# Kernel optimization log

Measured on AMD Instinct MI355X. Metric: run time of the kernel, lower is better.

Reference implementation:

```python
import jax, jax.numpy as jnp
import numpy as np
from jax import lax

HID = 512
NEG = -1e30

def conv2d(x, w, pad):
    # x: [N,C,H,W], w: [O,I,kh,kw]
    return lax.conv_general_dilated(x, w, (1, 1), [(pad, pad), (pad, pad)],
                                    dimension_numbers=('NCHW', 'OIHW', 'NCHW'))

def maxpool3s2p1(x):
    return lax.reduce_window(x, -jnp.inf, lax.max, (1, 1, 3, 3), (1, 1, 2, 2),
                             [(0, 0), (0, 0), (1, 1), (1, 1)])

def setup_inputs() -> dict:
    key = jax.random.key(0)
    ks = jax.random.split(key, 12)
    N, B = 128, 16
    gid = jnp.repeat(jnp.arange(B), N // B).astype(jnp.float32)  # sorted group ids
    rois = jnp.concatenate([gid[:, None], jax.random.uniform(ks[0], (N, 4))], axis=1)
    interact_feat = jax.random.normal(ks[1], (N, 2304, 1, 16, 16), jnp.float32)
    bbox_feat = jax.random.normal(ks[2], (N, 1024, 4, 7, 7), jnp.float32)
    s = lambda k, sh: jax.random.normal(k, sh, jnp.float32) * 0.02
    return {
        'rois': rois,
        'interact_feat': interact_feat,
        'bbox_feat': bbox_feat,
        'w_reduce': s(ks[3], (HID, 2304, 1, 1)),
        'w_rsize': s(ks[4], (HID, HID, 3, 3)),
        'wq': s(ks[5], (HID, HID, 3, 3)),
        'wk': s(ks[6], (HID, HID, 3, 3)),
        'wv': s(ks[7], (HID, HID, 3, 3)),
        'w1': s(ks[8], (HID, HID, 3, 3)),
        'gamma': jnp.ones((HID,), jnp.float32),
        'beta': jnp.zeros((HID,), jnp.float32),
        'w_fc': s(ks[9], (HID, 2 * HID)),
    }

def reference(rois, interact_feat, bbox_feat, w_reduce, w_rsize, wq, wk, wv, w1, gamma, beta, w_fc):
    f = interact_feat[:, :, 0]                      # squeeze(2): [N,2304,16,16]
    f = jax.nn.relu(conv2d(f, w_reduce, 0))         # [N,512,16,16]
    f = conv2d(f, w_rsize, 0)                       # no padding -> [N,512,14,14]
    f = maxpool3s2p1(f)                             # [N,512,7,7]

    gid = rois[:, 0].astype(jnp.int32)
    mask = gid[:, None] == gid[None, :]             # [N,N] same-group mask (vectorizes ragged loop)

    q = conv2d(f, wq, 1)
    k = conv2d(f, wk, 1)
    v = conv2d(f, wv, 1)
    # per-pixel attention across rois within each group
    att = jnp.einsum('ichw,jchw->ijhw', q, k) / jnp.sqrt(jnp.asarray(HID, f.dtype))
    att = jnp.where(mask[:, :, None, None], att, NEG)
    att = jax.nn.softmax(att, axis=1)               # softmax over key rois (dim=1)
    virt = jnp.einsum('ijhw,jchw->ichw', att, v)    # [N,512,7,7]

    # GroupNorm(1, C): normalize over (C,H,W), per-channel affine
    mu = virt.mean(axis=(1, 2, 3), keepdims=True)
    var = virt.var(axis=(1, 2, 3), keepdims=True)
    virt = (virt - mu) / jnp.sqrt(var + 1e-5)
    virt = virt * gamma[None, :, None, None] + beta[None, :, None, None]
    virt = jax.nn.relu(virt)
    virt = conv2d(virt, w1, 1)                      # dropout = identity in eval

    ho = (f + virt).mean(axis=(2, 3))               # gap1 -> [N,512]
    ob = bbox_feat.mean(axis=(2, 3, 4))             # gap2 -> [N,1024]
    ob = jax.nn.relu(ob @ w_fc.T)                   # fc1 -> [N,512]
    return jnp.concatenate([ho, ob], axis=1)        # [N,1024]
```

## Files before the change

### kernel.cpp

```cpp
#include <hip/hip_runtime.h>
#include <hip/hip_bf16.h>
#include <math.h>

typedef __bf16 bf16;
typedef __bf16 v8bf __attribute__((ext_vector_type(8)));
typedef float f32x4 __attribute__((ext_vector_type(4)));

#define GLDS16(g, l) __builtin_amdgcn_global_load_lds( \
    (const __attribute__((address_space(1))) void*)(g), \
    (__attribute__((address_space(3))) void*)(l), 16, 0, 0)

__device__ __forceinline__ int xcd_swz(int bid, int nwg) {
  int xcd = bid & 7, off = bid >> 3;
  int q = nwg >> 3, r = nwg & 7;
  return (xcd < r ? xcd * (q + 1) : r * (q + 1) + (xcd - r) * q) + off;
}

__device__ __forceinline__ void tile_compute(const char* ldsA, const char* ldsB,
                                             f32x4 (&acc)[4][4], int wr, int wc, int lane) {
  const int l15 = lane & 15;
  const int colb = (lane >> 4) << 4;
  #pragma unroll
  for (int kk = 0; kk < 2; ++kk) {
    v8bf a[4], b[4];
    #pragma unroll
    for (int i = 0; i < 4; ++i) {
      int ra = wr * 64 + i * 16 + l15;
      int ca = ((kk << 6) | colb) ^ ((ra & 7) << 4);
      a[i] = *(const v8bf*)(ldsA + ra * 128 + ca);
    }
    #pragma unroll
    for (int j = 0; j < 4; ++j) {
      int rb = wc * 64 + j * 16 + l15;
      int cb = ((kk << 6) | colb) ^ ((rb & 7) << 4);
      b[j] = *(const v8bf*)(ldsB + rb * 128 + cb);
    }
    __builtin_amdgcn_s_setprio(1);
    #pragma unroll
    for (int i = 0; i < 4; ++i)
      #pragma unroll
      for (int j = 0; j < 4; ++j)
        acc[i][j] = __builtin_amdgcn_mfma_f32_16x16x32_bf16(a[i], b[j], acc[i][j], 0, 0, 0);
    __builtin_amdgcn_s_setprio(0);
  }
}

#define PIPELINE_LOOP(NK)                                                   \
  stage(0, lds);                                                            \
  stage(1, lds + 32768);                                                    \
  int cur = 0;                                                              \
  for (int ks = 0; ks < (NK) - 1; ++ks) {                                   \
    asm volatile("s_waitcnt vmcnt(8)" ::: "memory");                        \
    __builtin_amdgcn_s_barrier();                                           \
    __builtin_amdgcn_sched_barrier(0);                                      \
    tile_compute(lds + cur * 32768, lds + cur * 32768 + 16384, acc, wr, wc, lane); \
    __builtin_amdgcn_sched_barrier(0);                                      \
    __builtin_amdgcn_s_barrier();                                           \
    __builtin_amdgcn_sched_barrier(0);                                      \
    if (ks + 2 < (NK)) stage(ks + 2, lds + cur * 32768);                    \
    cur ^= 1;                                                               \
  }                                                                         \
  asm volatile("s_waitcnt vmcnt(0)" ::: "memory");                          \
  __builtin_amdgcn_s_barrier();                                             \
  __builtin_amdgcn_sched_barrier(0);                                        \
  tile_compute(lds + cur * 32768, lds + cur * 32768 + 16384, acc, wr, wc, lane);

template<typename OutT, bool RELU>
__device__ __forceinline__ void store_tile(OutT* __restrict__ C, int m0, int c0,
                                           f32x4 (&acc)[4][4], int lane) {
  const int rbase = (lane >> 4) << 2;
  const int cl = lane & 15;
  #pragma unroll
  for (int i = 0; i < 4; ++i)
    #pragma unroll
    for (int j = 0; j < 4; ++j)
      #pragma unroll
      for (int r = 0; r < 4; ++r) {
        float v = acc[i][j][r];
        if (RELU) v = fmaxf(v, 0.f);
        C[(size_t)(m0 + i * 16 + rbase + r) * 512 + (c0 + j * 16 + cl)] = (OutT)v;
      }
}

__global__ __launch_bounds__(256)
void k_gemm_reduce(const bf16* __restrict__ A, const bf16* __restrict__ B,
                   bf16* __restrict__ f1, int mbase)
{
  __shared__ __attribute__((aligned(16))) char lds[65536];
  const int s = xcd_swz(blockIdx.x, gridDim.x);
  const int by = s & 3, bx = s >> 2;
  const int t = threadIdx.x, lane = t & 63, w = t >> 6, wr = w >> 1, wc = w & 1;
  const int tr = t >> 3;
  const int cphys = ((t & 7) << 4) ^ ((tr & 7) << 4);
  const char* pa[4]; const char* pb[4];
  #pragma unroll
  for (int i = 0; i < 4; ++i) {
    int r = i * 32 + tr;
    pa[i] = (const char*)A + (size_t)(bx * 128 + r) * 4608 + cphys;
    pb[i] = (const char*)B + (size_t)(by * 128 + r) * 4608 + cphys;
  }
  const int lo = t * 16;
  auto stage = [&](int ks, char* base) {
    #pragma unroll
    for (int i = 0; i < 4; ++i) GLDS16(pa[i] + ks * 128, base + lo + i * 4096);
    #pragma unroll
    for (int i = 0; i < 4; ++i) GLDS16(pb[i] + ks * 128, base + 16384 + lo + i * 4096);
  };
  f32x4 acc[4][4] = {};
  PIPELINE_LOOP(36)
  store_tile<bf16, true>(f1, mbase + bx * 128 + wr * 64, by * 128 + wc * 64, acc, lane);
}

__global__ __launch_bounds__(256)
void k_conv_rsize(const bf16* __restrict__ f1, const bf16* __restrict__ wt,
                  bf16* __restrict__ f14)
{
  __shared__ __attribute__((aligned(16))) char lds[65536];
  const int s = xcd_swz(blockIdx.x, gridDim.x);
  const int by = s & 3, bx = s >> 2;
  const int t = threadIdx.x, lane = t & 63, w = t >> 6, wr = w >> 1, wc = w & 1;
  const int tr = t >> 3;
  const int cphys = ((t & 7) << 4) ^ ((tr & 7) << 4);
  int abase[4]; const char* pb[4];
  #pragma unroll
  for (int i = 0; i < 4; ++i) {
    int r = i * 32 + tr;
    int m = bx * 128 + r;
    int n = m / 196, rem = m - n * 196;
    int y = rem / 14, x = rem - 14 * (rem / 14);
    abase[i] = n * 256 + y * 16 + x;
    pb[i] = (const char*)wt + (size_t)(by * 128 + r) * 1024 + cphys;
  }
  const char* f1c = (const char*)f1 + cphys;
  const int lo = t * 16;
  auto stage = [&](int ks, char* base) {
    int tap = ks >> 3, ko = (ks & 7) << 7;
    int dy = (tap * 11) >> 5, dx = tap - dy * 3;
    int doff = dy * 16 + dx;
    #pragma unroll
    for (int i = 0; i < 4; ++i)
      GLDS16(f1c + ((size_t)(abase[i] + doff) << 10) + ko, base + lo + i * 4096);
    #pragma unroll
    for (int i = 0; i < 4; ++i)
      GLDS16(pb[i] + (size_t)tap * 524288 + ko, base + 16384 + lo + i * 4096);
  };
  f32x4 acc[4][4] = {};
  PIPELINE_LOOP(72)
  store_tile<bf16, false>(f14, bx * 128 + wr * 64, by * 128 + wc * 64, acc, lane);
}

__global__ __launch_bounds__(256)
void k_conv_qkv(const bf16* __restrict__ fin, const bf16* __restrict__ wt,
                bf16* __restrict__ qkv, const bf16* __restrict__ zp,
                const float* __restrict__ bbox, float* __restrict__ obm)
{
  __shared__ __attribute__((aligned(16))) char lds[65536];
  const int t = threadIdx.x;
  if (blockIdx.x >= 588) {
    int bid = blockIdx.x - 588;
    int n = bid >> 4;
    int c = (bid & 15) * 64 + (t >> 2);
    int seg = t & 3;
    const float4* p4 = (const float4*)(bbox + ((size_t)n * 1024 + c) * 196);
    float s = 0.f;
    for (int k = seg; k < 49; k += 4) { float4 w = p4[k]; s += w.x + w.y + w.z + w.w; }
    s += __shfl_xor(s, 1);
    s += __shfl_xor(s, 2);
    if (seg == 0) obm[n * 1024 + c] = s * (1.f / 196.f);
    return;
  }
  const int s = xcd_swz(blockIdx.x, 588);
  const int q12 = s % 12, bx = s / 12;
  const int tensor = q12 >> 2, by = q12 & 3;
  const char* wtc = (const char*)wt + (size_t)tensor * 4718592;
  bf16* outp = qkv + (size_t)tensor * 3211264;
  const int lane = t & 63, w = t >> 6, wr = w >> 1, wc = w & 1;
  const int tr = t >> 3;
  const int cphys = ((t & 7) << 4) ^ ((tr & 7) << 4);
  int nb[4], py[4], px[4]; const char* pb[4];
  #pragma unroll
  for (int i = 0; i < 4; ++i) {
    int r = i * 32 + tr;
    int m = bx * 128 + r;
    int n = m / 49, rem = m - n * 49;
    nb[i] = n * 49;
    py[i] = rem / 7 - 1;
    px[i] = rem - 7 * (rem / 7) - 1;
    pb[i] = wtc + (size_t)(by * 128 + r) * 1024 + cphys;
  }
  const char* finc = (const char*)fin + cphys;
  const char* zpc = (const char*)zp;
  const int lo = t * 16;
  auto stage = [&](int ks, char* base) {
    int tap = ks >> 3, ko = (ks & 7) << 7;
    int dy = (tap * 11) >> 5, dx = tap - dy * 3;
    #pragma unroll
    for (int i = 0; i < 4; ++i) {
      int iy = py[i] + dy, ix = px[i] + dx;
      const char* src = ((unsigned)iy < 7u && (unsigned)ix < 7u)
          ? finc + ((size_t)(nb[i] + iy * 7 + ix) << 10) + ko : zpc;
      GLDS16(src, base + lo + i * 4096);
    }
    #pragma unroll
    for (int i = 0; i < 4; ++i)
      GLDS16(pb[i] + (size_t)tap * 524288 + ko, base + 16384 + lo + i * 4096);
  };
  f32x4 acc[4][4] = {};
  PIPELINE_LOOP(72)
  store_tile<bf16, false>(outp, bx * 128 + wr * 64, by * 128 + wc * 64, acc, lane);
}

__global__ __launch_bounds__(256)
void k_gemm_s(const bf16* __restrict__ A_s, const bf16* __restrict__ w1r,
              float* __restrict__ part)
{
  __shared__ __attribute__((aligned(16))) char lds[65536];
  const int by = blockIdx.x, kspl = blockIdx.y;
  const int t = threadIdx.x, lane = t & 63, w = t >> 6, wr = w >> 1, wc = w & 1;
  const int tr = t >> 3;
  const int cphys = ((t & 7) << 4) ^ ((tr & 7) << 4);
  const char* pa[4]; const char* pb[4];
  #pragma unroll
  for (int i = 0; i < 4; ++i) {
    int r = i * 32 + tr;
    pa[i] = (const char*)A_s + (size_t)r * 9216 + kspl * 2304 + cphys;
    pb[i] = (const char*)w1r + (size_t)(by * 128 + r) * 9216 + kspl * 2304 + cphys;
  }
  const int lo = t * 16;
  auto stage = [&](int ks, char* base) {
    #pragma unroll
    for (int i = 0; i < 4; ++i) GLDS16(pa[i] + ks * 128, base + lo + i * 4096);
    #pragma unroll
    for (int i = 0; i < 4; ++i) GLDS16(pb[i] + ks * 128, base + 16384 + lo + i * 4096);
  };
  f32x4 acc[4][4] = {};
  PIPELINE_LOOP(18)
  const int rb = (lane >> 4) << 2, cl = lane & 15;
  #pragma unroll
  for (int i = 0; i < 4; ++i)
    #pragma unroll
    for (int j = 0; j < 4; ++j)
      #pragma unroll
      for (int r = 0; r < 4; ++r) {
        int row = wr * 64 + i * 16 + rb + r;
        int col = by * 128 + wc * 64 + j * 16 + cl;
        part[(size_t)kspl * 65536 + row * 512 + col] = acc[i][j][r];
      }
}

__global__ __launch_bounds__(512)
void k_red(const float* __restrict__ part, const float* __restrict__ f7m,
           float* __restrict__ out)
{
  int idx = blockIdx.x * 512 + threadIdx.x;
  float s = part[idx] + part[65536 + idx] + part[131072 + idx] + part[196608 + idx];
  int row = idx >> 9, col = idx & 511;
  out[row * 1024 + col] = s + f7m[idx];
}

__global__ void k_tin(const float* __restrict__ in, bf16* __restrict__ A1, int n0)
{
  __shared__ float tile[64][36];
  const int k0 = blockIdx.x * 64, p0 = blockIdx.y * 32, nl = blockIdx.z;
  const int n = n0 + nl;
  const int t = threadIdx.x;
  const float* src = in + (size_t)n * 2304 * 256;
  #pragma unroll
  for (int rep = 0; rep < 2; ++rep) {
    int idx = t + rep * 256;
    int row = idx >> 3, c4 = (idx & 7) * 4;
    float4 v = *(const float4*)(src + (size_t)(k0 + row) * 256 + p0 + c4);
    tile[row][c4] = v.x; tile[row][c4 + 1] = v.y;
    tile[row][c4 + 2] = v.z; tile[row][c4 + 3] = v.w;
  }
  __syncthreads();
  const int pl = t >> 3, ke = (t & 7) * 8;
  v8bf o;
  #pragma unroll
  for (int e = 0; e < 8; ++e) o[e] = (bf16)tile[ke + e][pl];
  bf16* dst = A1 + (size_t)nl * 256 * 2304;
  *(v8bf*)(dst + (size_t)(p0 + pl) * 2304 + k0 + ke) = o;
}

__global__ void k_castw(const float* __restrict__ wsrc, bf16* __restrict__ wb, int nelem)
{
  int idx = (blockIdx.x * 256 + threadIdx.x) * 4;
  if (idx >= nelem) return;
  float4 v = *(const float4*)(wsrc + idx);
  bf16 o0 = (bf16)v.x, o1 = (bf16)v.y, o2 = (bf16)v.z, o3 = (bf16)v.w;
  bf16* d = wb + idx;
  d[0] = o0; d[1] = o1; d[2] = o2; d[3] = o3;
}

__global__ void k_wtrans(const float* __restrict__ s0, const float* __restrict__ s1,
                         const float* __restrict__ s2, const float* __restrict__ s3,
                         const float* __restrict__ s4, bf16* __restrict__ wt,
                         bf16* __restrict__ w1r)
{
  const float* src;
  switch (blockIdx.y) {
    case 0: src = s0; break; case 1: src = s1; break; case 2: src = s2; break;
    case 3: src = s3; break; default: src = s4; break;
  }
  int q = blockIdx.x * 256 + threadIdx.x;
  const float* sp = src + (size_t)q * 9;
  float tmp[9];
  #pragma unroll
  for (int e = 0; e < 9; ++e) tmp[e] = sp[e];
  if (blockIdx.y < 4) {
    bf16* dst = wt + (size_t)blockIdx.y * 2359296;
    #pragma unroll
    for (int e = 0; e < 9; ++e) dst[(size_t)e * 262144 + q] = (bf16)tmp[e];
  } else {
    int co = q >> 9, ci = q & 511;
    #pragma unroll
    for (int e = 0; e < 9; ++e) w1r[(size_t)(co * 9 + e) * 512 + ci] = (bf16)tmp[e];
  }
}

__global__ void k_pool(const bf16* __restrict__ f14, bf16* __restrict__ f7b)
{
  int idx = blockIdx.x * 256 + threadIdx.x;
  int c2 = idx & 255;
  int pp = idx >> 8;
  int n = pp / 49, p7 = pp - n * 49;
  int y = p7 / 7, x = p7 - 7 * (p7 / 7);
  int y0 = 2 * y - 1, x0 = 2 * x - 1;
  const unsigned* f14u = (const unsigned*)f14;
  float m0 = -3.4e38f, m1 = -3.4e38f;
  #pragma unroll
  for (int dy = 0; dy < 3; ++dy) {
    int iy = y0 + dy; if ((unsigned)iy >= 14u) continue;
    #pragma unroll
    for (int dx = 0; dx < 3; ++dx) {
      int ix = x0 + dx; if ((unsigned)ix >= 14u) continue;
      unsigned vv = f14u[(size_t)(n * 196 + iy * 14 + ix) * 256 + c2];
      m0 = fmaxf(m0, __builtin_bit_cast(float, vv << 16));
      m1 = fmaxf(m1, __builtin_bit_cast(float, vv & 0xffff0000u));
    }
  }
  bf16 b0 = (bf16)m0, b1 = (bf16)m1;
  unsigned pk = (unsigned)__builtin_bit_cast(unsigned short, b0)
              | ((unsigned)__builtin_bit_cast(unsigned short, b1) << 16);
  ((unsigned*)f7b)[idx] = pk;
}

__global__ __launch_bounds__(256)
void k_attn(const bf16* __restrict__ q, const bf16* __restrict__ k,
            const bf16* __restrict__ v, const float* __restrict__ rois,
            float* __restrict__ virt)
{
  const int p = blockIdx.x, g = blockIdx.y, t = threadIdx.x;
  __shared__ float sS[8][9];
  __shared__ float sP[8][9];
  __shared__ __attribute__((aligned(16))) bf16 sV[8][512];
  {
    int u = t;
    #pragma unroll
    for (int rep = 0; rep < 2; ++rep, u += 256) {
      int j = u >> 6, ch = u & 63;
      *(v8bf*)&sV[j][ch * 8] = *(const v8bf*)(v + ((size_t)(g * 8 + j) * 49 + p) * 512 + ch * 8);
    }
  }
  int pi = t >> 2, ls = t & 3;
  int i = pi >> 3, j = pi & 7;
  const bf16* qi = q + ((size_t)(g * 8 + i) * 49 + p) * 512;
  const bf16* kj = k + ((size_t)(g * 8 + j) * 49 + p) * 512;
  float s = 0.f;
  for (int ch = ls * 16; ch < ls * 16 + 16; ++ch) {
    v8bf a = *(const v8bf*)(qi + ch * 8);
    v8bf b = *(const v8bf*)(kj + ch * 8);
    #pragma unroll
    for (int e = 0; e < 8; ++e) s += (float)a[e] * (float)b[e];
  }
  s += __shfl_xor(s, 1);
  s += __shfl_xor(s, 2);
  if (ls == 0) sS[i][j] = s * 0.04419417382415922f;
  __syncthreads();
  if (t < 8) {
    float gi = rois[(g * 8 + t) * 5];
    float pv[8]; float mx = -3.4e38f;
    #pragma unroll
    for (int jj = 0; jj < 8; ++jj) {
      float gj = rois[(g * 8 + jj) * 5];
      float sv = (gi == gj) ? sS[t][jj] : -1e30f;
      pv[jj] = sv; mx = fmaxf(mx, sv);
    }
    float sum = 0.f;
    #pragma unroll
    for (int jj = 0; jj < 8; ++jj) { float e = expf(pv[jj] - mx); pv[jj] = e; sum += e; }
    float inv = 1.f / sum;
    #pragma unroll
    for (int jj = 0; jj < 8; ++jj) sP[t][jj] = pv[jj] * inv;
  }
  __syncthreads();
  int i2 = t >> 5, c0 = (t & 31) * 16;
  float o[16];
  #pragma unroll
  for (int e = 0; e < 16; ++e) o[e] = 0.f;
  #pragma unroll
  for (int jj = 0; jj < 8; ++jj) {
    float ww = sP[i2][jj];
    v8bf v0 = *(const v8bf*)&sV[jj][c0];
    v8bf v1 = *(const v8bf*)&sV[jj][c0 + 8];
    #pragma unroll
    for (int e = 0; e < 8; ++e) { o[e] += ww * (float)v0[e]; o[8 + e] += ww * (float)v1[e]; }
  }
  float* dst = virt + ((size_t)(g * 8 + i2) * 49 + p) * 512 + c0;
  #pragma unroll
  for (int e = 0; e < 16; ++e) dst[e] = o[e];
}

__global__ __launch_bounds__(512)
void k_ln_fc(const float* __restrict__ virt, const float* __restrict__ gamma,
             const float* __restrict__ beta, const bf16* __restrict__ f7b,
             bf16* __restrict__ A_s, float* __restrict__ f7m,
             const float* __restrict__ obm, const float* __restrict__ wfc,
             float* __restrict__ out)
{
  const int t = threadIdx.x;
  if (blockIdx.x >= 128) {
    __shared__ float sO[1024];
    int n = blockIdx.x - 128;
    for (int u = t; u < 1024; u += 512) sO[u] = obm[n * 1024 + u];
    __syncthreads();
    const float4* wp = (const float4*)(wfc + (size_t)t * 1024);
    float s = 0.f;
    for (int c4 = 0; c4 < 256; ++c4) {
      float4 w = wp[c4];
      s += w.x * sO[c4 * 4] + w.y * sO[c4 * 4 + 1] + w.z * sO[c4 * 4 + 2] + w.w * sO[c4 * 4 + 3];
    }
    out[n * 1024 + 512 + t] = fmaxf(s, 0.f);
    return;
  }
  const int n = blockIdx.x;
  const float* p = virt + (size_t)n * 25088 + t;
  float xv[49];
  float s1 = 0.f, s2 = 0.f;
  #pragma unroll
  for (int pp = 0; pp < 49; ++pp) {
    float x = p[pp * 512];
    xv[pp] = x; s1 += x; s2 += x * x;
  }
  __shared__ float r1[512], r2[512];
  r1[t] = s1; r2[t] = s2; __syncthreads();
  for (int off = 256; off; off >>= 1) {
    if (t < off) { r1[t] += r1[t + off]; r2[t] += r2[t + off]; }
    __syncthreads();
  }
  float mu = r1[0] * (1.f / 25088.f);
  float var = r2[0] * (1.f / 25088.f) - mu * mu;
  float rstd = rsqrtf(var + 1e-5f);
  float g = gamma[t], be = beta[t];
  const bf16* fp = f7b + (size_t)n * 25088 + t;
  float T = 0, R0 = 0, R6 = 0, C0 = 0, C6 = 0;
  float X00 = 0, X06 = 0, X60 = 0, X66 = 0, F = 0;
  #pragma unroll
  for (int pp = 0; pp < 49; ++pp) {
    const int u = pp / 7, v = pp - 7 * (pp / 7);
    float y = fmaxf((xv[pp] - mu) * rstd * g + be, 0.f);
    T += y;
    if (u == 0) R0 += y;
    if (u == 6) R6 += y;
    if (v == 0) C0 += y;
    if (v == 6) C6 += y;
    if (pp == 0)  X00 = y;
    if (pp == 6)  X06 = y;
    if (pp == 42) X60 = y;
    if (pp == 48) X66 = y;
    F += (float)fp[pp * 512];
  }
  float sv[9] = { T-R6-C6+X66, T-R6, T-R6-C0+X60,
                  T-C6,        T,    T-C0,
                  T-R0-C6+X06, T-R0, T-R0-C0+X00 };
  bf16* Ap = A_s + (size_t)n * 4608 + t;
  #pragma unroll
  for (int tap = 0; tap < 9; ++tap)
    Ap[tap * 512] = (bf16)(sv[tap] * (1.f / 49.f));
  f7m[n * 512 + t] = F * (1.f / 49.f);
}

extern "C" void kernel_launch(void* const* d_in, const int* in_sizes, int n_in,
                              void* d_out, int out_size, void* d_ws, size_t ws_size,
                              hipStream_t stream) {
  const float* rois     = (const float*)d_in[0];
  const float* interact = (const float*)d_in[1];
  const float* bbox     = (const float*)d_in[2];
  const float* w_reduce = (const float*)d_in[3];
  const float* w_rsize  = (const float*)d_in[4];
  const float* wq       = (const float*)d_in[5];
  const float* wk       = (const float*)d_in[6];
  const float* wv       = (const float*)d_in[7];
  const float* w1       = (const float*)d_in[8];
  const float* gamma    = (const float*)d_in[9];
  const float* beta     = (const float*)d_in[10];
  const float* wfc      = (const float*)d_in[11];
  float* out = (float*)d_out;
  char* ws = (char*)d_ws;

  size_t o = 0;
  auto take = [&](size_t sz) { size_t r = o; o += (sz + 255) & ~(size_t)255; return r; };
  bf16*  wrb   = (bf16*)(ws + take(2359296));
  bf16*  wt    = (bf16*)(ws + take(18874368));
  bf16*  w1r   = (bf16*)(ws + take(4718592));
  char*  Rf1   = ws + take(33554432);
  bf16*  f7b   = (bf16*)(ws + take(6422528));
  float* virt  = (float*)(ws + take(12845056));
  bf16*  A_s   = (bf16*)(ws + take(1179648));
  float* f7m   = (float*)(ws + take(262144));
  float* part  = (float*)(ws + take(1048576));
  float* obm   = (float*)(ws + take(524288));
  bf16*  zp    = (bf16*)(ws + take(256));
  size_t fixedEnd = o;
  const size_t A1_FULL = 150994944;
  bool full = (ws_size >= fixedEnd + A1_FULL);
  bf16* A1  = (bf16*)(ws + fixedEnd);
  bf16* f14 = (bf16*)(ws + fixedEnd);

  bf16* f1 = (bf16*)Rf1;
  bf16* qb = (bf16*)Rf1;
  bf16* kb = qb + 3211264;
  bf16* vb = kb + 3211264;

  hipMemsetAsync(zp, 0, 256, stream);

  k_castw<<<1152, 256, 0, stream>>>(w_reduce, wrb, 1179648);
  k_wtrans<<<dim3(1024, 5), 256, 0, stream>>>(w_rsize, wq, wk, wv, w1, wt, w1r);

  if (full) {
    k_tin<<<dim3(36, 8, 128), 256, 0, stream>>>(interact, A1, 0);
    k_gemm_reduce<<<1024, 256, 0, stream>>>(A1, wrb, f1, 0);
  } else {
    for (int ch = 0; ch < 4; ++ch) {
      k_tin<<<dim3(36, 8, 32), 256, 0, stream>>>(interact, A1, ch * 32);
      k_gemm_reduce<<<256, 256, 0, stream>>>(A1, wrb, f1, ch * 8192);
    }
  }

  k_conv_rsize<<<784, 256, 0, stream>>>(f1, wt, f14);
  k_pool<<<6272, 256, 0, stream>>>(f14, f7b);

  k_conv_qkv<<<2636, 256, 0, stream>>>(f7b, wt + (size_t)1 * 2359296, qb, zp, bbox, obm);

  k_attn<<<dim3(49, 16), 256, 0, stream>>>(qb, kb, vb, rois, virt);

  k_ln_fc<<<256, 512, 0, stream>>>(virt, gamma, beta, f7b, A_s, f7m, obm, wfc, out);

  k_gemm_s<<<dim3(4, 4), 256, 0, stream>>>(A_s, w1r, part);
  k_red<<<128, 512, 0, stream>>>(part, f7m, out);
}
```

Baseline: 552.1 us.

## Switch main GEMM/conv kernels to 256x256 tiles with 8 waves and 4-stage ring

```diff
diff --git a/kernel.cpp b/kernel.cpp
--- a/kernel.cpp
+++ b/kernel.cpp
@@ -14,6 +14,229 @@
   int xcd = bid & 7, off = bid >> 3;
   int q = nwg >> 3, r = nwg & 7;
   return (xcd < r ? xcd * (q + 1) : r * (q + 1) + (xcd - r) * q) + off;
+}
+
+#define LDA256(ih) do { \
+  _Pragma("unroll") for (int _i = 0; _i < 4; ++_i) { \
+    int _r = (ih) * 64 + _i * 16 + l15; \
+    int _c = (wm * 64 + colb) ^ ((l15 & 7) << 4); \
+    af[_i] = *(const v8bf*)(ringp + _r * 128 + _c); } } while (0)
+
+#define LDB256() do { \
+  _Pragma("unroll") for (int _j = 0; _j < 4; ++_j) { \
+    int _r = (wn & 1) * 64 + _j * 16 + l15; \
+    int _c = ((wn >> 1) * 64 + colb) ^ ((l15 & 7) << 4); \
+    bfr[_j] = *(const v8bf*)(ringp + 16384 + _r * 128 + _c); } } while (0)
+
+#define MMA256(ih) do { \
+  __builtin_amdgcn_s_setprio(1); \
+  _Pragma("unroll") for (int _i = 0; _i < 4; ++_i) \
+  _Pragma("unroll") for (int _j = 0; _j < 4; ++_j) \
+    acc[(ih)*4+_i][_j] = __builtin_amdgcn_mfma_f32_16x16x32_bf16(af[_i], bfr[_j], acc[(ih)*4+_i][_j], 0, 0, 0); \
+  __builtin_amdgcn_s_setprio(0); } while (0)
+
+#define GROUP256(g, NT, STAGEA, STAGEB) do { \
+  const char* ringp = lds + ((g) & 3) * 32768; \
+  char* srng = lds + (((g) + 3) & 3) * 32768; \
+  (void)srng; \
+  const bool _st = ((g) + 3 < (NT)); \
+  LDA256(0); LDB256(); \
+  if (_st) { STAGEA; } \
+  __builtin_amdgcn_s_barrier(); \
+  __builtin_amdgcn_sched_barrier(0); \
+  MMA256(0); \
+  __builtin_amdgcn_sched_barrier(0); \
+  __builtin_amdgcn_s_barrier(); \
+  LDA256(1); \
+  if (_st) { STAGEB; } \
+  if (_st)                       asm volatile("s_waitcnt vmcnt(8)" ::: "memory"); \
+  else if ((g) + 3 == (NT))      asm volatile("s_waitcnt vmcnt(4)" ::: "memory"); \
+  else if ((g) + 3 == (NT) + 1)  asm volatile("s_waitcnt vmcnt(0)" ::: "memory"); \
+  __builtin_amdgcn_s_barrier(); \
+  __builtin_amdgcn_sched_barrier(0); \
+  MMA256(1); \
+  __builtin_amdgcn_sched_barrier(0); \
+  __builtin_amdgcn_s_barrier(); } while (0)
+
+__global__ __launch_bounds__(512, 2)
+void k_gemm_reduce(const bf16* __restrict__ A, const bf16* __restrict__ B,
+                   bf16* __restrict__ f1, int mbase)
+{
+  __shared__ __attribute__((aligned(16))) char lds[131072];
+  const int s = xcd_swz(blockIdx.x, gridDim.x);
+  const int by = s & 1, bx = s >> 1;
+  const int t = threadIdx.x, lane = t & 63, w = t >> 6;
+  const int wm = w >> 2, wn = w & 3;
+  const int l15 = lane & 15, colb = (lane >> 4) << 4;
+  const int tr = t >> 3;
+  const int lb = ((t & 7) << 4) ^ ((tr & 7) << 4);
+  const int hi = lb >> 6, kb = lb & 63;
+  const int t16 = t * 16;
+  const char* pa[2]; const char* pb[2];
+  #pragma unroll
+  for (int j = 0; j < 2; ++j) {
+    pa[j] = (const char*)A + (size_t)(bx * 256 + j * 64 + tr + hi * 128) * 4608 + kb;
+    pb[j] = (const char*)B + (size_t)(by * 256 + j * 64 + tr + hi * 128) * 4608 + kb;
+  }
+  #define SA_GR(kt, ring) do { GLDS16(pa[0]+(size_t)(kt)*64, (ring)+t16); \
+                               GLDS16(pa[1]+(size_t)(kt)*64, (ring)+8192+t16); } while (0)
+  #define SB_GR(kt, ring) do { GLDS16(pb[0]+(size_t)(kt)*64, (ring)+16384+t16); \
+                               GLDS16(pb[1]+(size_t)(kt)*64, (ring)+24576+t16); } while (0)
+  f32x4 acc[8][4] = {};
+  v8bf af[4], bfr[4];
+  SA_GR(0, lds);         SB_GR(0, lds);
+  SA_GR(1, lds + 32768); SB_GR(1, lds + 32768);
+  SA_GR(2, lds + 65536); SB_GR(2, lds + 65536);
+  asm volatile("s_waitcnt vmcnt(8)" ::: "memory");
+  __builtin_amdgcn_s_barrier();
+  for (int g = 0; g < 72; ++g) {
+    GROUP256(g, 72, SA_GR(g + 3, srng), SB_GR(g + 3, srng));
+  }
+  const int rbase = (lane >> 4) << 2, cl = lane & 15;
+  #pragma unroll
+  for (int i = 0; i < 8; ++i)
+    #pragma unroll
+    for (int j = 0; j < 4; ++j)
+      #pragma unroll
+      for (int r = 0; r < 4; ++r) {
+        int row = mbase + bx * 256 + wm * 128 + i * 16 + rbase + r;
+        int col = by * 256 + wn * 64 + j * 16 + cl;
+        f1[(size_t)row * 512 + col] = (bf16)fmaxf(acc[i][j][r], 0.f);
+      }
+}
+
+__global__ __launch_bounds__(512, 2)
+void k_conv_rsize(const bf16* __restrict__ f1, const bf16* __restrict__ wt,
+                  bf16* __restrict__ f14)
+{
+  __shared__ __attribute__((aligned(16))) char lds[131072];
+  const int s = xcd_swz(blockIdx.x, gridDim.x);
+  const int by = s & 1, bx = s >> 1;
+  const int t = threadIdx.x, lane = t & 63, w = t >> 6;
+  const int wm = w >> 2, wn = w & 3;
+  const int l15 = lane & 15, colb = (lane >> 4) << 4;
+  const int tr = t >> 3;
+  const int lb = ((t & 7) << 4) ^ ((tr & 7) << 4);
+  const int hi = lb >> 6, kb = lb & 63;
+  const int t16 = t * 16;
+  int abase[2]; const char* pb[2];
+  #pragma unroll
+  for (int j = 0; j < 2; ++j) {
+    int m = bx * 256 + j * 64 + tr + hi * 128;
+    int n = m / 196, rem = m - n * 196;
+    int y = rem / 14, x = rem - 14 * (rem / 14);
+    abase[j] = n * 256 + y * 16 + x;
+    pb[j] = (const char*)wt + (size_t)(by * 256 + j * 64 + tr + hi * 128) * 1024 + kb;
+  }
+  const char* f1c = (const char*)f1 + kb;
+  #define SA_CR(kt, ring) do { int _tap = (kt) >> 4, _ko = ((kt) & 15) << 6; \
+    int _dy = (_tap * 11) >> 5, _dx = _tap - _dy * 3; int _df = _dy * 16 + _dx; \
+    GLDS16(f1c + (size_t)(abase[0] + _df) * 1024 + _ko, (ring)+t16); \
+    GLDS16(f1c + (size_t)(abase[1] + _df) * 1024 + _ko, (ring)+8192+t16); } while (0)
+  #define SB_CR(kt, ring) do { int _tap = (kt) >> 4, _ko = ((kt) & 15) << 6; \
+    GLDS16(pb[0] + (size_t)_tap * 524288 + _ko, (ring)+16384+t16); \
+    GLDS16(pb[1] + (size_t)_tap * 524288 + _ko, (ring)+24576+t16); } while (0)
+  f32x4 acc[8][4] = {};
+  v8bf af[4], bfr[4];
+  SA_CR(0, lds);         SB_CR(0, lds);
+  SA_CR(1, lds + 32768); SB_CR(1, lds + 32768);
+  SA_CR(2, lds + 65536); SB_CR(2, lds + 65536);
+  asm volatile("s_waitcnt vmcnt(8)" ::: "memory");
+  __builtin_amdgcn_s_barrier();
+  for (int g = 0; g < 144; ++g) {
+    GROUP256(g, 144, SA_CR(g + 3, srng), SB_CR(g + 3, srng));
+  }
+  const int rbase = (lane >> 4) << 2, cl = lane & 15;
+  #pragma unroll
+  for (int i = 0; i < 8; ++i)
+    #pragma unroll
+    for (int j = 0; j < 4; ++j)
+      #pragma unroll
+      for (int r = 0; r < 4; ++r) {
+        int row = bx * 256 + wm * 128 + i * 16 + rbase + r;
+        int col = by * 256 + wn * 64 + j * 16 + cl;
+        f14[(size_t)row * 512 + col] = (bf16)acc[i][j][r];
+      }
+}
+
+__global__ __launch_bounds__(512, 2)
+void k_conv_qkv(const bf16* __restrict__ fin, const bf16* __restrict__ wt,
+                bf16* __restrict__ qkv, const bf16* __restrict__ zp,
+                const float* __restrict__ bbox, float* __restrict__ obm)
+{
+  __shared__ __attribute__((aligned(16))) char lds[131072];
+  const int t = threadIdx.x;
+  if (blockIdx.x >= 150) {
+    int bid = blockIdx.x - 150;
+    int n = bid >> 3;
+    int c = (bid & 7) * 128 + (t >> 2);
+    int seg = t & 3;
+    const float4* p4 = (const float4*)(bbox + ((size_t)n * 1024 + c) * 196);
+    float sum = 0.f;
+    for (int k = seg; k < 49; k += 4) { float4 ww = p4[k]; sum += ww.x + ww.y + ww.z + ww.w; }
+    sum += __shfl_xor(sum, 1);
+    sum += __shfl_xor(sum, 2);
+    if (seg == 0) obm[n * 1024 + c] = sum * (1.f / 196.f);
+    return;
+  }
+  const int s = xcd_swz(blockIdx.x, 150);
+  const int q6 = s % 6, bx = s / 6;
+  const int tensor = q6 >> 1, byl = q6 & 1;
+  const char* wtc = (const char*)wt + (size_t)tensor * 4718592;
+  bf16* outp = qkv + (size_t)tensor * 3211264;
+  const int lane = t & 63, w = t >> 6;
+  const int wm = w >> 2, wn = w & 3;
+  const int l15 = lane & 15, colb = (lane >> 4) << 4;
+  const int tr = t >> 3;
+  const int lb = ((t & 7) << 4) ^ ((tr & 7) << 4);
+  const int hi = lb >> 6, kb = lb & 63;
+  const int t16 = t * 16;
+  int nb[2], py[2], px[2]; const char* pb[2];
+  #pragma unroll
+  for (int j = 0; j < 2; ++j) {
+    int m = bx * 256 + j * 64 + tr + hi * 128;
+    if (m > 6271) m = 6271;
+    int n = m / 49, rem = m - n * 49;
+    nb[j] = n * 49;
+    py[j] = rem / 7 - 1;
+    px[j] = rem - 7 * (rem / 7) - 1;
+    pb[j] = wtc + (size_t)(byl * 256 + j * 64 + tr + hi * 128) * 1024 + kb;
+  }
+  const char* finc = (const char*)fin + kb;
+  const char* zpc = (const char*)zp;
+  #define SA_QK(kt, ring) do { int _tap = (kt) >> 4, _ko = ((kt) & 15) << 6; \
+    int _dy = (_tap * 11) >> 5, _dx = _tap - _dy * 3; \
+    _Pragma("unroll") for (int _j = 0; _j < 2; ++_j) { \
+      int _iy = py[_j] + _dy, _ix = px[_j] + _dx; \
+      const char* _sp = ((unsigned)_iy < 7u && (unsigned)_ix < 7u) \
+          ? finc + (size_t)(nb[_j] + _iy * 7 + _ix) * 1024 + _ko : zpc; \
+      GLDS16(_sp, (ring) + _j * 8192 + t16); } } while (0)
+  #define SB_QK(kt, ring) do { int _tap = (kt) >> 4, _ko = ((kt) & 15) << 6; \
+    GLDS16(pb[0] + (size_t)_tap * 524288 + _ko, (ring)+16384+t16); \
+    GLDS16(pb[1] + (size_t)_tap * 524288 + _ko, (ring)+24576+t16); } while (0)
+  f32x4 acc[8][4] = {};
+  v8bf af[4], bfr[4];
+  SA_QK(0, lds);         SB_QK(0, lds);
+  SA_QK(1, lds + 32768); SB_QK(1, lds + 32768);
+  SA_QK(2, lds + 65536); SB_QK(2, lds + 65536);
+  asm volatile("s_waitcnt vmcnt(8)" ::: "memory");
+  __builtin_amdgcn_s_barrier();
+  for (int g = 0; g < 144; ++g) {
+    GROUP256(g, 144, SA_QK(g + 3, srng), SB_QK(g + 3, srng));
+  }
+  const int rbase = (lane >> 4) << 2, cl = lane & 15;
+  #pragma unroll
+  for (int i = 0; i < 8; ++i)
+    #pragma unroll
+    for (int j = 0; j < 4; ++j)
+      #pragma unroll
+      for (int r = 0; r < 4; ++r) {
+        int row = bx * 256 + wm * 128 + i * 16 + rbase + r;
+        if (row < 6272) {
+          int col = byl * 256 + wn * 64 + j * 16 + cl;
+          outp[(size_t)row * 512 + col] = (bf16)acc[i][j][r];
+        }
+      }
 }
 
 __device__ __forceinline__ void tile_compute(const char* ldsA, const char* ldsB,
@@ -65,151 +288,6 @@
   __builtin_amdgcn_sched_barrier(0);                                        \
   tile_compute(lds + cur * 32768, lds + cur * 32768 + 16384, acc, wr, wc, lane);
 
-template<typename OutT, bool RELU>
-__device__ __forceinline__ void store_tile(OutT* __restrict__ C, int m0, int c0,
-                                           f32x4 (&acc)[4][4], int lane) {
-  const int rbase = (lane >> 4) << 2;
-  const int cl = lane & 15;
-  #pragma unroll
-  for (int i = 0; i < 4; ++i)
-    #pragma unroll
-    for (int j = 0; j < 4; ++j)
-      #pragma unroll
-      for (int r = 0; r < 4; ++r) {
-        float v = acc[i][j][r];
-        if (RELU) v = fmaxf(v, 0.f);
-        C[(size_t)(m0 + i * 16 + rbase + r) * 512 + (c0 + j * 16 + cl)] = (OutT)v;
-      }
-}
-
-__global__ __launch_bounds__(256)
-void k_gemm_reduce(const bf16* __restrict__ A, const bf16* __restrict__ B,
-                   bf16* __restrict__ f1, int mbase)
-{
-  __shared__ __attribute__((aligned(16))) char lds[65536];
-  const int s = xcd_swz(blockIdx.x, gridDim.x);
-  const int by = s & 3, bx = s >> 2;
-  const int t = threadIdx.x, lane = t & 63, w = t >> 6, wr = w >> 1, wc = w & 1;
-  const int tr = t >> 3;
-  const int cphys = ((t & 7) << 4) ^ ((tr & 7) << 4);
-  const char* pa[4]; const char* pb[4];
-  #pragma unroll
-  for (int i = 0; i < 4; ++i) {
-    int r = i * 32 + tr;
-    pa[i] = (const char*)A + (size_t)(bx * 128 + r) * 4608 + cphys;
-    pb[i] = (const char*)B + (size_t)(by * 128 + r) * 4608 + cphys;
-  }
-  const int lo = t * 16;
-  auto stage = [&](int ks, char* base) {
-    #pragma unroll
-    for (int i = 0; i < 4; ++i) GLDS16(pa[i] + ks * 128, base + lo + i * 4096);
-    #pragma unroll
-    for (int i = 0; i < 4; ++i) GLDS16(pb[i] + ks * 128, base + 16384 + lo + i * 4096);
-  };
-  f32x4 acc[4][4] = {};
-  PIPELINE_LOOP(36)
-  store_tile<bf16, true>(f1, mbase + bx * 128 + wr * 64, by * 128 + wc * 64, acc, lane);
-}
-
-__global__ __launch_bounds__(256)
-void k_conv_rsize(const bf16* __restrict__ f1, const bf16* __restrict__ wt,
-                  bf16* __restrict__ f14)
-{
-  __shared__ __attribute__((aligned(16))) char lds[65536];
-  const int s = xcd_swz(blockIdx.x, gridDim.x);
-  const int by = s & 3, bx = s >> 2;
-  const int t = threadIdx.x, lane = t & 63, w = t >> 6, wr = w >> 1, wc = w & 1;
-  const int tr = t >> 3;
-  const int cphys = ((t & 7) << 4) ^ ((tr & 7) << 4);
-  int abase[4]; const char* pb[4];
-  #pragma unroll
-  for (int i = 0; i < 4; ++i) {
-    int r = i * 32 + tr;
-    int m = bx * 128 + r;
-    int n = m / 196, rem = m - n * 196;
-    int y = rem / 14, x = rem - 14 * (rem / 14);
-    abase[i] = n * 256 + y * 16 + x;
-    pb[i] = (const char*)wt + (size_t)(by * 128 + r) * 1024 + cphys;
-  }
-  const char* f1c = (const char*)f1 + cphys;
-  const int lo = t * 16;
-  auto stage = [&](int ks, char* base) {
-    int tap = ks >> 3, ko = (ks & 7) << 7;
-    int dy = (tap * 11) >> 5, dx = tap - dy * 3;
-    int doff = dy * 16 + dx;
-    #pragma unroll
-    for (int i = 0; i < 4; ++i)
-      GLDS16(f1c + ((size_t)(abase[i] + doff) << 10) + ko, base + lo + i * 4096);
-    #pragma unroll
-    for (int i = 0; i < 4; ++i)
-      GLDS16(pb[i] + (size_t)tap * 524288 + ko, base + 16384 + lo + i * 4096);
-  };
-  f32x4 acc[4][4] = {};
-  PIPELINE_LOOP(72)
-  store_tile<bf16, false>(f14, bx * 128 + wr * 64, by * 128 + wc * 64, acc, lane);
-}
-
-__global__ __launch_bounds__(256)
-void k_conv_qkv(const bf16* __restrict__ fin, const bf16* __restrict__ wt,
-                bf16* __restrict__ qkv, const bf16* __restrict__ zp,
-                const float* __restrict__ bbox, float* __restrict__ obm)
-{
-  __shared__ __attribute__((aligned(16))) char lds[65536];
-  const int t = threadIdx.x;
-  if (blockIdx.x >= 588) {
-    int bid = blockIdx.x - 588;
-    int n = bid >> 4;
-    int c = (bid & 15) * 64 + (t >> 2);
-    int seg = t & 3;
-    const float4* p4 = (const float4*)(bbox + ((size_t)n * 1024 + c) * 196);
-    float s = 0.f;
-    for (int k = seg; k < 49; k += 4) { float4 w = p4[k]; s += w.x + w.y + w.z + w.w; }
-    s += __shfl_xor(s, 1);
-    s += __shfl_xor(s, 2);
-    if (seg == 0) obm[n * 1024 + c] = s * (1.f / 196.f);
-    return;
-  }
-  const int s = xcd_swz(blockIdx.x, 588);
-  const int q12 = s % 12, bx = s / 12;
-  const int tensor = q12 >> 2, by = q12 & 3;
-  const char* wtc = (const char*)wt + (size_t)tensor * 4718592;
-  bf16* outp = qkv + (size_t)tensor * 3211264;
-  const int lane = t & 63, w = t >> 6, wr = w >> 1, wc = w & 1;
-  const int tr = t >> 3;
-  const int cphys = ((t & 7) << 4) ^ ((tr & 7) << 4);
-  int nb[4], py[4], px[4]; const char* pb[4];
-  #pragma unroll
-  for (int i = 0; i < 4; ++i) {
-    int r = i * 32 + tr;
-    int m = bx * 128 + r;
-    int n = m / 49, rem = m - n * 49;
-    nb[i] = n * 49;
-    py[i] = rem / 7 - 1;
-    px[i] = rem - 7 * (rem / 7) - 1;
-    pb[i] = wtc + (size_t)(by * 128 + r) * 1024 + cphys;
-  }
-  const char* finc = (const char*)fin + cphys;
-  const char* zpc = (const char*)zp;
-  const int lo = t * 16;
-  auto stage = [&](int ks, char* base) {
-    int tap = ks >> 3, ko = (ks & 7) << 7;
-    int dy = (tap * 11) >> 5, dx = tap - dy * 3;
-    #pragma unroll
-    for (int i = 0; i < 4; ++i) {
-      int iy = py[i] + dy, ix = px[i] + dx;
-      const char* src = ((unsigned)iy < 7u && (unsigned)ix < 7u)
-          ? finc + ((size_t)(nb[i] + iy * 7 + ix) << 10) + ko : zpc;
-      GLDS16(src, base + lo + i * 4096);
-    }
-    #pragma unroll
-    for (int i = 0; i < 4; ++i)
-      GLDS16(pb[i] + (size_t)tap * 524288 + ko, base + 16384 + lo + i * 4096);
-  };
-  f32x4 acc[4][4] = {};
-  PIPELINE_LOOP(72)
-  store_tile<bf16, false>(outp, bx * 128 + wr * 64, by * 128 + wc * 64, acc, lane);
-}
-
 __global__ __launch_bounds__(256)
 void k_gemm_s(const bf16* __restrict__ A_s, const bf16* __restrict__ w1r,
               float* __restrict__ part)
@@ -529,18 +607,18 @@
 
   if (full) {
     k_tin<<<dim3(36, 8, 128), 256, 0, stream>>>(interact, A1, 0);
-    k_gemm_reduce<<<1024, 256, 0, stream>>>(A1, wrb, f1, 0);
+    k_gemm_reduce<<<256, 512, 0, stream>>>(A1, wrb, f1, 0);
   } else {
     for (int ch = 0; ch < 4; ++ch) {
       k_tin<<<dim3(36, 8, 32), 256, 0, stream>>>(interact, A1, ch * 32);
-      k_gemm_reduce<<<256, 256, 0, stream>>>(A1, wrb, f1, ch * 8192);
+      k_gemm_reduce<<<64, 512, 0, stream>>>(A1, wrb, f1, ch * 8192);
     }
   }
 
-  k_conv_rsize<<<784, 256, 0, stream>>>(f1, wt, f14);
+  k_conv_rsize<<<196, 512, 0, stream>>>(f1, wt, f14);
   k_pool<<<6272, 256, 0, stream>>>(f14, f7b);
 
-  k_conv_qkv<<<2636, 256, 0, stream>>>(f7b, wt + (size_t)1 * 2359296, qb, zp, bbox, obm);
+  k_conv_qkv<<<1174, 512, 0, stream>>>(f7b, wt + (size_t)1 * 2359296, qb, zp, bbox, obm);
 
   k_attn<<<dim3(49, 16), 256, 0, stream>>>(qb, kb, vb, rois, virt);
 
```

After: 551.4 us. No clear change (-0.1%).
